# Kernel tuning notes

Measured on AMD Instinct MI355X. Metric: run time of the kernel, lower is better.

## Reference

```python
import jax, jax.numpy as jnp
import numpy as np

B, N, C, S, G, COOR = 4, 8192, 64, 2048, 32, 3
C2 = 2 * C            # channels after SetAbstraction
EXP = 4
RADII = (0.2, 0.4, 0.4)


def _sqdist(src, dst):
    # (B,M,3),(B,N,3) -> (B,M,N) squared distances (same expansion as torch code)
    d = -2.0 * jnp.einsum('bmc,bnc->bmn', src, dst)
    d = d + jnp.sum(src ** 2, -1)[:, :, None]
    d = d + jnp.sum(dst ** 2, -1)[:, None, :]
    return d


def _gather(points, idx):
    # points (B,N,C), idx (B,...) -> (B,...,C)
    return jax.vmap(lambda p, i: p[i])(points, idx)


def _fps(xyz, npoint):
    # xyz (B,N,3) -> (B,npoint) farthest point sample indices (start at index 0)
    b, n, _ = xyz.shape

    def step(carry, _):
        distance, farthest = carry
        centroid = jnp.take_along_axis(xyz, farthest[:, None, None], axis=1)  # (B,1,3)
        d = jnp.sqrt(jnp.sum((xyz - centroid) ** 2, -1))
        distance = jnp.minimum(distance, d)
        nxt = jnp.argmax(distance, -1)
        return (distance, nxt), farthest

    init = (jnp.full((b, n), 1e10, xyz.dtype), jnp.zeros((b,), jnp.int32))
    _, idxs = jax.lax.scan(step, init, None, length=npoint)
    return jnp.transpose(idxs)  # (B,npoint)


def _query_hybrid(radius, nsample, xyz, new_xyz):
    d = _sqdist(new_xyz, xyz)                       # (B,S,N)
    neg_d, idx = jax.lax.top_k(-d, nsample)         # smallest distances
    mask = (-neg_d) > radius ** 2
    first = idx[:, :, :1]
    return jnp.where(mask, first, idx)              # (B,S,nsample)


def _group(coor, new_coor, fea, radius, nsample):
    # coor (B,N,3), new_coor (B,S,3), fea (B,N,C) -> (B,S,G,C+3)
    gi = _query_hybrid(radius, nsample, coor, new_coor)
    gc = (_gather(coor, gi) - new_coor[:, :, None, :]) / radius
    gf = _gather(fea, gi)
    return jnp.concatenate([gf, gc], axis=-1)


def _mlp_max(g, w):
    # g (B,S,G,Cin), w (Cout,Cin): 1x1 conv (no bias) + ReLU, then max over group
    h = jax.nn.relu(jnp.einsum('bsgc,dc->bsgd', g, w))
    return jnp.max(h, axis=2)  # (B,S,Cout)


def _inv_res_mlp(coor, fea, radius, nsample, w_la, w1, w2):
    # coor (B,S,3), fea (B,S,C2) channels-last
    identity = fea
    g = _group(coor, coor, fea, radius, nsample)
    fea = _mlp_max(g, w_la)                              # LocalAggregation
    fea = jax.nn.relu(jnp.einsum('bsc,dc->bsd', fea, w1))
    fea = jnp.einsum('bsc,dc->bsd', fea, w2)             # last ReLU dropped
    return jax.nn.relu(fea + identity)


def setup_inputs() -> dict:
    key = jax.random.key(0)
    ks = jax.random.split(key, 10)
    def w(k, o, i):
        return jax.random.normal(k, (o, i), jnp.float32) / np.sqrt(i)
    return {
        'points_coor': jax.random.uniform(ks[0], (B, 3, N), jnp.float32),
        'points_fea': jax.random.normal(ks[1], (B, C, N), jnp.float32),
        'w_sa':  w(ks[2], C2, C + COOR),
        'w_la1': w(ks[3], C2, C2 + COOR),
        'w1_1':  w(ks[4], C2 * EXP, C2),
        'w2_1':  w(ks[5], C2, C2 * EXP),
        'w_la2': w(ks[6], C2, C2 + COOR),
        'w1_2':  w(ks[7], C2 * EXP, C2),
        'w2_2':  w(ks[8], C2, C2 * EXP),
    }


def reference(points_coor, points_fea, w_sa, w_la1, w1_1, w2_1, w_la2, w1_2, w2_2):
    coor = jnp.transpose(points_coor, (0, 2, 1))  # (B,N,3)
    fea = jnp.transpose(points_fea, (0, 2, 1))    # (B,N,C)
    # SetAbstraction: S-G-P
    fps_idx = _fps(coor, S)
    new_coor = _gather(coor, fps_idx)             # (B,S,3)
    g = _group(coor, new_coor, fea, RADII[0], G)
    new_fea = _mlp_max(g, w_sa)                   # (B,S,2C)
    # InvResMLP blocks
    new_fea = _inv_res_mlp(new_coor, new_fea, RADII[1], G, w_la1, w1_1, w2_1)
    new_fea = _inv_res_mlp(new_coor, new_fea, RADII[2], G, w_la2, w1_2, w2_2)
    return (jnp.transpose(new_coor, (0, 2, 1)), jnp.transpose(new_fea, (0, 2, 1)))
```

## Files before the change

kernel.cpp:

```cpp
#include <hip/hip_runtime.h>
#include <hip/hip_bf16.h>

#define BB 4
#define NN 8192
#define CC 64
#define SS 2048
#define GG 32
#define C2V 128
#define HHV 512

typedef unsigned long long u64;
typedef unsigned int u32;

__global__ void k_transpose_fea(const float* __restrict__ in, float* __restrict__ out) {
  __shared__ float tile[32][33];
  const int b = blockIdx.z;
  const int n0 = blockIdx.x * 32, c0 = blockIdx.y * 32;
  const int tx = threadIdx.x, ty = threadIdx.y;
  const float* src = in + (size_t)b * CC * NN;
#pragma unroll
  for (int i = 0; i < 32; i += 8)
    tile[ty + i][tx] = src[(size_t)(c0 + ty + i) * NN + n0 + tx];
  __syncthreads();
  float* dst = out + (size_t)b * NN * CC;
#pragma unroll
  for (int i = 0; i < 32; i += 8)
    dst[(size_t)(n0 + ty + i) * CC + c0 + tx] = tile[tx][ty + i];
}

__global__ __launch_bounds__(512) void k_fps(const float* __restrict__ pc, int* __restrict__ fps_idx) {
#pragma clang fp contract(off)
  const int b = blockIdx.x, tid = threadIdx.x;
  const int lane = tid & 63, wid = tid >> 6;
  const float* pb = pc + (size_t)b * 3 * NN;
  const float4* p4x = (const float4*)pb;
  const float4* p4y = (const float4*)(pb + NN);
  const float4* p4z = (const float4*)(pb + 2 * NN);
  float4 X0 = p4x[tid * 4 + 0], X1 = p4x[tid * 4 + 1], X2 = p4x[tid * 4 + 2], X3 = p4x[tid * 4 + 3];
  float4 Y0 = p4y[tid * 4 + 0], Y1 = p4y[tid * 4 + 1], Y2 = p4y[tid * 4 + 2], Y3 = p4y[tid * 4 + 3];
  float4 Z0 = p4z[tid * 4 + 0], Z1 = p4z[tid * 4 + 1], Z2 = p4z[tid * 4 + 2], Z3 = p4z[tid * 4 + 3];
  float4 D0 = make_float4(1e20f, 1e20f, 1e20f, 1e20f);
  float4 D1 = D0, D2q = D0, D3 = D0;

  __shared__ u64 sK[2][8];
  if (lane == 0)
    sK[0][wid] = (wid == 0) ? ((((u64)0xFFFFFFFFu) << 32) | (u64)0xFFFFFFFFu) : 0ull;
  __syncthreads();

#define DPPK64(K, CTL) { \
      u32 lo = (u32)(K), hi = (u32)((K) >> 32); \
      u32 lo2 = (u32)__builtin_amdgcn_update_dpp(0, (int)lo, CTL, 0xf, 0xf, false); \
      u32 hi2 = (u32)__builtin_amdgcn_update_dpp(0, (int)hi, CTL, 0xf, 0xf, false); \
      u64 k2 = ((u64)hi2 << 32) | (u64)lo2; if (k2 > (K)) (K) = k2; }
#define RMAXF(V, CTL) { \
      float t_ = __int_as_float(__builtin_amdgcn_update_dpp(0, __float_as_int(V), CTL, 0xf, 0xf, false)); \
      (V) = fmaxf((V), t_); }
#define RMINU(V, CTL) { \
      u32 t_ = (u32)__builtin_amdgcn_update_dpp(0, (int)(V), CTL, 0xf, 0xf, false); \
      (V) = min((V), t_); }

  for (int k = 0; k < SS; ++k) {
    const int p = k & 1;
    u64 kk = sK[p][lane & 7];
    DPPK64(kk, 0x121) DPPK64(kk, 0x122) DPPK64(kk, 0x124)
    const int g = (int)(0xFFFFFFFFu - (u32)kk);
    if (tid == 0) fps_idx[b * SS + k] = g;
    const float cx = pb[g], cy = pb[NN + g], cz = pb[2 * NN + g];

#define UPDC(XX, YY, ZZ, DD) { \
      float dx_ = (XX) - cx, dy_ = (YY) - cy, dz_ = (ZZ) - cz; \
      float t0_ = dx_ * dx_, t1_ = dy_ * dy_, t2_ = dz_ * dz_; \
      float s_ = (t0_ + t1_) + t2_; \
      (DD) = fminf((DD), s_); }
    UPDC(X0.x, Y0.x, Z0.x, D0.x) UPDC(X0.y, Y0.y, Z0.y, D0.y)
    UPDC(X0.z, Y0.z, Z0.z, D0.z) UPDC(X0.w, Y0.w, Z0.w, D0.w)
    UPDC(X1.x, Y1.x, Z1.x, D1.x) UPDC(X1.y, Y1.y, Z1.y, D1.y)
    UPDC(X1.z, Y1.z, Z1.z, D1.z) UPDC(X1.w, Y1.w, Z1.w, D1.w)
    UPDC(X2.x, Y2.x, Z2.x, D2q.x) UPDC(X2.y, Y2.y, Z2.y, D2q.y)
    UPDC(X2.z, Y2.z, Z2.z, D2q.z) UPDC(X2.w, Y2.w, Z2.w, D2q.w)
    UPDC(X3.x, Y3.x, Z3.x, D3.x) UPDC(X3.y, Y3.y, Z3.y, D3.y)
    UPDC(X3.z, Y3.z, Z3.z, D3.z) UPDC(X3.w, Y3.w, Z3.w, D3.w)
#undef UPDC

    float m2 = fmaxf(
        fmaxf(fmaxf(fmaxf(D0.x, D0.y), fmaxf(D0.z, D0.w)),
              fmaxf(fmaxf(D1.x, D1.y), fmaxf(D1.z, D1.w))),
        fmaxf(fmaxf(fmaxf(D2q.x, D2q.y), fmaxf(D2q.z, D2q.w)),
              fmaxf(fmaxf(D3.x, D3.y), fmaxf(D3.z, D3.w))));
    float s = sqrtf(m2);

    u32 sbits = __float_as_uint(s);
    float spred = __uint_as_float(sbits - 1u);
    double M = ((double)spred + (double)s) * 0.5;
    double L = M * M;
    if (sbits & 1u) L = __longlong_as_double(__double_as_longlong(L) + 1ll);
    float Lf = (float)L;
    if ((double)Lf < L) Lf = __uint_as_float(__float_as_uint(Lf) + 1u);

    int jsel = 0;
    jsel = (D3.w >= Lf) ? 15 : jsel; jsel = (D3.z >= Lf) ? 14 : jsel;
    jsel = (D3.y >= Lf) ? 13 : jsel; jsel = (D3.x >= Lf) ? 12 : jsel;
    jsel = (D2q.w >= Lf) ? 11 : jsel; jsel = (D2q.z >= Lf) ? 10 : jsel;
    jsel = (D2q.y >= Lf) ? 9 : jsel; jsel = (D2q.x >= Lf) ? 8 : jsel;
    jsel = (D1.w >= Lf) ? 7 : jsel; jsel = (D1.z >= Lf) ? 6 : jsel;
    jsel = (D1.y >= Lf) ? 5 : jsel; jsel = (D1.x >= Lf) ? 4 : jsel;
    jsel = (D0.w >= Lf) ? 3 : jsel; jsel = (D0.z >= Lf) ? 2 : jsel;
    jsel = (D0.y >= Lf) ? 1 : jsel; jsel = (D0.x >= Lf) ? 0 : jsel;

    float sm = s;
    RMAXF(sm, 0x121) RMAXF(sm, 0x122) RMAXF(sm, 0x124) RMAXF(sm, 0x128)
    sm = fmaxf(sm, __shfl_xor(sm, 16, 64));
    sm = fmaxf(sm, __shfl_xor(sm, 32, 64));
    u32 enc = (s == sm) ? (u32)(tid * 16 + jsel) : 0xFFFFFFFFu;
    RMINU(enc, 0x121) RMINU(enc, 0x122) RMINU(enc, 0x124) RMINU(enc, 0x128)
    enc = min(enc, (u32)__shfl_xor((int)enc, 16, 64));
    enc = min(enc, (u32)__shfl_xor((int)enc, 32, 64));

    u64 key = (((u64)__float_as_uint(sm)) << 32) | (u64)(0xFFFFFFFFu - enc);
    if (lane == 0) sK[p ^ 1][wid] = key;
    __syncthreads();
  }
#undef DPPK64
#undef RMAXF
#undef RMINU
}

__global__ void k_gather(const float* __restrict__ pc, const int* __restrict__ fps_idx,
                         float* __restrict__ ncoor, float* __restrict__ out0) {
  int t = blockIdx.x * 256 + threadIdx.x;
  if (t >= BB * SS) return;
  int b = t / SS, s = t % SS;
  int id = fps_idx[t];
  const float* base = pc + (size_t)b * 3 * NN;
  float x = base[id], y = base[NN + id], z = base[2 * NN + id];
  ncoor[(size_t)t * 3] = x; ncoor[(size_t)t * 3 + 1] = y; ncoor[(size_t)t * 3 + 2] = z;
  size_t o = (size_t)b * 3 * SS + s;
  out0[o] = x; out0[o + SS] = y; out0[o + 2 * SS] = z;
}

__global__ __launch_bounds__(256) void k_knn(const float* __restrict__ candp,
                                             const float* __restrict__ newc,
                                             int mode, int ncand, float r2,
                                             int* __restrict__ gidx) {
  __shared__ float cd[2048];
  __shared__ int ci[2048];
  __shared__ int hist[64];
  __shared__ int cnt, oc, binT, mlow;
  const int q = blockIdx.x, tid = threadIdx.x;
  const int b = q / SS;
  if (tid == 0) { cnt = 0; oc = 0; }
  if (tid < 64) hist[tid] = 0;
  __syncthreads();
  const float qx = newc[(size_t)q * 3], qy = newc[(size_t)q * 3 + 1], qz = newc[(size_t)q * 3 + 2];
  float qn;
  {
#pragma clang fp contract(off)
    qn = (qx * qx + qy * qy) + qz * qz;
  }
  const float sc = 64.0f / r2;
  const float* base = (mode == 0) ? candp + (size_t)b * 3 * NN : candp + (size_t)b * SS * 3;
  for (int i = tid; i < ncand; i += 256) {
    float x, y, z;
    if (mode == 0) { x = base[i]; y = base[NN + i]; z = base[2 * NN + i]; }
    else { x = base[3 * i]; y = base[3 * i + 1]; z = base[3 * i + 2]; }
    float dot = fmaf(qz, z, fmaf(qy, y, qx * x));
    float d;
    {
#pragma clang fp contract(off)
      float pn = (x * x + y * y) + z * z;
      d = ((-2.0f * dot) + qn) + pn;
    }
    if (d <= r2) {
      int pp = atomicAdd(&cnt, 1);
      if (pp < 2048) { cd[pp] = d; ci[pp] = i; }
      float db = (d > 0.0f) ? d : 0.0f;
      atomicAdd(&hist[min(63, (int)(db * sc))], 1);
    }
  }
  __syncthreads();
  const int M = min(cnt, 2048);
  if (tid == 0) {
    if (M > 32) {
      int c = 0, t = 0;
      for (t = 0; t < 64; ++t) { if (c + hist[t] >= 32) break; c += hist[t]; }
      binT = t; mlow = c;
    } else binT = -1;
  }
  __syncthreads();
  int* out = gidx + (size_t)q * 32;
  if (binT < 0) {
    for (int j = tid; j < M; j += 256) out[atomicAdd(&oc, 1)] = ci[j];
    __syncthreads();
    if (tid == 0 && M < 32) {
      float bd = 1e30f; int bx = 0x7FFFFFFF;
      for (int j = 0; j < M; ++j)
        if (cd[j] < bd || (cd[j] == bd && ci[j] < bx)) { bd = cd[j]; bx = ci[j]; }
      for (int j = M; j < 32; ++j) out[j] = bx;
    }
  } else {
    const int bt = binT, m = mlow;
    for (int j = tid; j < M; j += 256) {
      float dbj = (cd[j] > 0.0f) ? cd[j] : 0.0f;
      int bin = min(63, (int)(dbj * sc));
      if (bin < bt) out[atomicAdd(&oc, 1)] = ci[j];
      else if (bin == bt) {
        int r = 0; const float dj = cd[j]; const int ij = ci[j];
        for (int kk = 0; kk < M; ++kk) {
          float dbk = (cd[kk] > 0.0f) ? cd[kk] : 0.0f;
          if (min(63, (int)(dbk * sc)) == bt &&
              (cd[kk] < dj || (cd[kk] == dj && ci[kk] < ij))) ++r;
        }
        if (m + r < 32) out[m + r] = ci[j];
      }
    }
  }
}

template <int FDIM>
__global__ __launch_bounds__(256) void k_group_mlp(
    const float* __restrict__ fea, const int* __restrict__ gidx,
    const float* __restrict__ newc, const float* __restrict__ candp,
    int mode, int ncand, float radius,
    const float* __restrict__ wp, float* __restrict__ outf) {
  constexpr int CP4 = FDIM + 4;
  constexpr int NC4 = CP4 / 4;
  __shared__ float4 g4[2][32][NC4];
  __shared__ int sidx[2][32];
  __shared__ float sq[2][3];
  __shared__ float pf[2][4][128];
  const int tid = threadIdx.x;
  const int rs = tid >> 7, tl = tid & 127;
  const int dt = tl & 31, et = tl >> 5;
  const int d0 = dt * 4, e0 = et * 8;
  const int row0 = blockIdx.x * 16;
  for (int rp = 0; rp < 16; rp += 2) {
    const int row = row0 + rp + rs;
    if (tl < 32) sidx[rs][tl] = gidx[(size_t)row * 32 + tl];
    if (tl < 3) sq[rs][tl] = newc[(size_t)row * 3 + tl];
    __syncthreads();
    const int bb2 = row / SS;
    const float* fb = fea + (size_t)bb2 * ncand * FDIM;
    const float* cb = (mode == 0) ? candp + (size_t)bb2 * 3 * NN
                                  : candp + (size_t)bb2 * SS * 3;
    float* gf = (float*)&g4[rs][0][0];
    for (int qq = tl; qq < 32 * CP4; qq += 128) {
      int e = qq / CP4, c = qq - e * CP4;
      int id = sidx[rs][e];
      float v;
      if (c < FDIM) v = fb[(size_t)id * FDIM + c];
      else if (c < FDIM + 3) {
        int comp = c - FDIM;
        float pcv = (mode == 0) ? cb[(size_t)comp * NN + id] : cb[(size_t)id * 3 + comp];
        v = (pcv - sq[rs][comp]) / radius;
      } else v = 0.0f;
      gf[qq] = v;
    }
    __syncthreads();
    float acc[4][8];
#pragma unroll
    for (int i = 0; i < 4; ++i)
#pragma unroll
      for (int j = 0; j < 8; ++j) acc[i][j] = 0.0f;
    const float4* w4 = (const float4*)wp;
    for (int c4 = 0; c4 < NC4; ++c4) {
      float4 wv[4], gv[8];
#pragma unroll
      for (int i = 0; i < 4; ++i) wv[i] = w4[(size_t)(d0 + i) * NC4 + c4];
#pragma unroll
      for (int j = 0; j < 8; ++j) gv[j] = g4[rs][e0 + j][c4];
#pragma unroll
      for (int i = 0; i < 4; ++i)
#pragma unroll
        for (int j = 0; j < 8; ++j) {
          acc[i][j] += wv[i].x * gv[j].x;
          acc[i][j] += wv[i].y * gv[j].y;
          acc[i][j] += wv[i].z * gv[j].z;
          acc[i][j] += wv[i].w * gv[j].w;
        }
    }
#pragma unroll
    for (int i = 0; i < 4; ++i) {
      float m = acc[i][0];
#pragma unroll
      for (int j = 1; j < 8; ++j) m = fmaxf(m, acc[i][j]);
      pf[rs][et][d0 + i] = m;
    }
    __syncthreads();
    {
      const int d = tid & 127, r2s = tid >> 7;
      const int rowW = row0 + rp + r2s;
      float m = fmaxf(fmaxf(pf[r2s][0][d], pf[r2s][1][d]),
                      fmaxf(pf[r2s][2][d], pf[r2s][3][d]));
      outf[(size_t)rowW * 128 + d] = fmaxf(m, 0.0f);
    }
    __syncthreads();
  }
}

template <bool RESID>
__global__ __launch_bounds__(256) void k_dense(
    const float* __restrict__ A, const float* __restrict__ W,
    const float* __restrict__ Id, float* __restrict__ Out,
    int K, int Ntot) {
  __shared__ float4 sa[64][17], sb[64][17];
  const int m0 = blockIdx.x * 64, n0 = blockIdx.y * 64;
  const int tid = threadIdx.x;
  const int mt = tid & 15, nt = tid >> 4;
  float acc[4][4];
#pragma unroll
  for (int i = 0; i < 4; ++i)
#pragma unroll
    for (int j = 0; j < 4; ++j) acc[i][j] = 0.0f;
  for (int kc = 0; kc < K; kc += 64) {
    for (int q2 = tid; q2 < 2048; q2 += 256) {
      int half = q2 >> 10, qq = q2 & 1023;
      int r = qq >> 4, c = qq & 15;
      const float* src = half ? (W + (size_t)(n0 + r) * K + kc + c * 4)
                              : (A + (size_t)(m0 + r) * K + kc + c * 4);
      float4 v = *(const float4*)src;
      if (half) sb[r][c] = v; else sa[r][c] = v;
    }
    __syncthreads();
#pragma unroll
    for (int c = 0; c < 16; ++c) {
      const int ks = (c + mt + nt) & 15;
      float4 av[4], bv[4];
#pragma unroll
      for (int i = 0; i < 4; ++i) av[i] = sa[mt * 4 + i][ks];
#pragma unroll
      for (int j = 0; j < 4; ++j) bv[j] = sb[nt * 4 + j][ks];
#pragma unroll
      for (int i = 0; i < 4; ++i)
#pragma unroll
        for (int j = 0; j < 4; ++j) {
          acc[i][j] += av[i].x * bv[j].x;
          acc[i][j] += av[i].y * bv[j].y;
          acc[i][j] += av[i].z * bv[j].z;
          acc[i][j] += av[i].w * bv[j].w;
        }
    }
    __syncthreads();
  }
#pragma unroll
  for (int i = 0; i < 4; ++i)
#pragma unroll
    for (int j = 0; j < 4; ++j) {
      size_t o = (size_t)(m0 + mt * 4 + i) * Ntot + n0 + nt * 4 + j;
      float v = acc[i][j];
      if (RESID) v += Id[o];
      Out[o] = fmaxf(v, 0.0f);
    }
}

__global__ void k_pad_w(const float* __restrict__ src, float* __restrict__ dst,
                        int rows, int cin, int cp4) {
  int t = blockIdx.x * 256 + threadIdx.x;
  if (t >= rows * cp4) return;
  int r = t / cp4, c = t - r * cp4;
  dst[t] = (c < cin) ? src[(size_t)r * cin + c] : 0.0f;
}

__global__ void k_out1_t(const float* __restrict__ in, float* __restrict__ out) {
  __shared__ float tile[32][33];
  const int b = blockIdx.z;
  const int s0 = blockIdx.x * 32, d0 = blockIdx.y * 32;
  const int tx = threadIdx.x, ty = threadIdx.y;
#pragma unroll
  for (int i = 0; i < 32; i += 8)
    tile[ty + i][tx] = in[(size_t)(b * SS + s0 + ty + i) * 128 + d0 + tx];
  __syncthreads();
#pragma unroll
  for (int i = 0; i < 32; i += 8)
    out[(size_t)(b * 128 + d0 + ty + i) * SS + s0 + tx] = tile[tx][ty + i];
}

extern "C" void kernel_launch(void* const* d_in, const int* in_sizes, int n_in,
                              void* d_out, int out_size, void* d_ws, size_t ws_size,
                              hipStream_t stream) {
  const float* pc    = (const float*)d_in[0];
  const float* pfea  = (const float*)d_in[1];
  const float* w_sa  = (const float*)d_in[2];
  const float* w_la1 = (const float*)d_in[3];
  const float* w1_1  = (const float*)d_in[4];
  const float* w2_1  = (const float*)d_in[5];
  const float* w_la2 = (const float*)d_in[6];
  const float* w1_2  = (const float*)d_in[7];
  const float* w2_2  = (const float*)d_in[8];
  float* out0 = (float*)d_out;
  float* out1 = out0 + (size_t)BB * 3 * SS;

  char* wsp = (char*)d_ws;
  size_t off = 0;
  auto alloc = [&](size_t bytes) -> void* {
    void* p = wsp + off;
    off = (off + bytes + 255) & ~(size_t)255;
    return p;
  };
  float* hbuf = (float*)alloc((size_t)BB * SS * HHV * 4);
  float* feaT = hbuf;
  int*   fpsi = (int*)alloc((size_t)BB * SS * 4);
  float* ncoor = (float*)alloc((size_t)BB * SS * 3 * 4);
  int*   gi = (int*)alloc((size_t)BB * SS * GG * 4);
  float* fa = (float*)alloc((size_t)BB * SS * C2V * 4);
  float* fb = (float*)alloc((size_t)BB * SS * C2V * 4);
  float* wsap = (float*)alloc(128 * 68 * 4);
  float* wla1p = (float*)alloc(128 * 132 * 4);
  float* wla2p = (float*)alloc(128 * 132 * 4);

  k_pad_w<<<dim3((128 * 68 + 255) / 256), dim3(256), 0, stream>>>(w_sa, wsap, 128, 67, 68);
  k_pad_w<<<dim3((128 * 132 + 255) / 256), dim3(256), 0, stream>>>(w_la1, wla1p, 128, 131, 132);
  k_pad_w<<<dim3((128 * 132 + 255) / 256), dim3(256), 0, stream>>>(w_la2, wla2p, 128, 131, 132);

  k_transpose_fea<<<dim3(NN / 32, CC / 32, BB), dim3(32, 8), 0, stream>>>(pfea, feaT);
  k_fps<<<dim3(BB), dim3(512), 0, stream>>>(pc, fpsi);
  k_gather<<<dim3((BB * SS + 255) / 256), dim3(256), 0, stream>>>(pc, fpsi, ncoor, out0);

  k_knn<<<dim3(BB * SS), dim3(256), 0, stream>>>(pc, ncoor, 0, NN, 0.04f, gi);
  k_group_mlp<64><<<dim3(BB * SS / 16), dim3(256), 0, stream>>>(feaT, gi, ncoor, pc, 0, NN, 0.2f, wsap, fa);

  k_knn<<<dim3(BB * SS), dim3(256), 0, stream>>>(ncoor, ncoor, 1, SS, 0.16f, gi);

  k_group_mlp<128><<<dim3(BB * SS / 16), dim3(256), 0, stream>>>(fa, gi, ncoor, ncoor, 1, SS, 0.4f, wla1p, fb);
  k_dense<false><<<dim3(128, 8), dim3(256), 0, stream>>>(fb, w1_1, nullptr, hbuf, 128, 512);
  k_dense<true><<<dim3(128, 2), dim3(256), 0, stream>>>(hbuf, w2_1, fa, fb, 512, 128);

  k_group_mlp<128><<<dim3(BB * SS / 16), dim3(256), 0, stream>>>(fb, gi, ncoor, ncoor, 1, SS, 0.4f, wla2p, fa);
  k_dense<false><<<dim3(128, 8), dim3(256), 0, stream>>>(fa, w1_2, nullptr, hbuf, 128, 512);
  k_dense<true><<<dim3(128, 2), dim3(256), 0, stream>>>(hbuf, w2_2, fb, fa, 512, 128);

  k_out1_t<<<dim3(SS / 32, 128 / 32, BB), dim3(32, 8), 0, stream>>>(fa, out1);
}
```

Baseline: 4.061 ms.

## Pass FPS winner coordinates via shared memory and compute sub-index only in winning lane

The FPS loop now has the winning thread of each wave write the selected point's coordinates and index into shared memory next to its key. Every lane then fetches the centroid with a shuffle instead of a dependent global load. The per-element argmax selection and threshold computation now run only in the lane holding the wave max, rather than in every lane before the reduction. The launch bounds also request two blocks per CU. This is meant to remove global-memory latency and redundant ALU work from the serial critical path, at the cost of divergent code in one lane and possible register pressure under the tighter launch bound.

```diff
diff --git a/kernel.cpp b/kernel.cpp
--- a/kernel.cpp
+++ b/kernel.cpp
@@ -28,7 +28,7 @@
     dst[(size_t)(n0 + ty + i) * CC + c0 + tx] = tile[tx][ty + i];
 }
 
-__global__ __launch_bounds__(512) void k_fps(const float* __restrict__ pc, int* __restrict__ fps_idx) {
+__global__ __launch_bounds__(512, 2) void k_fps(const float* __restrict__ pc, int* __restrict__ fps_idx) {
 #pragma clang fp contract(off)
   const int b = blockIdx.x, tid = threadIdx.x;
   const int lane = tid & 63, wid = tid >> 6;
@@ -43,8 +43,12 @@
   float4 D1 = D0, D2q = D0, D3 = D0;
 
   __shared__ u64 sK[2][8];
-  if (lane == 0)
-    sK[0][wid] = (wid == 0) ? ((((u64)0xFFFFFFFFu) << 32) | (u64)0xFFFFFFFFu) : 0ull;
+  __shared__ float4 sC[2][8];
+  if (lane == 0) sK[0][wid] = 0ull;
+  if (tid == 0) {
+    sK[0][0] = ~0ull;
+    sC[0][0] = make_float4(X0.x, Y0.x, Z0.x, __int_as_float(0));
+  }
   __syncthreads();
 
 #define DPPK64(K, CTL) { \
@@ -60,12 +64,16 @@
       (V) = min((V), t_); }
 
   for (int k = 0; k < SS; ++k) {
-    const int p = k & 1;
+    const int p = k & 1, pn = p ^ 1;
     u64 kk = sK[p][lane & 7];
+    float4 cw = sC[p][lane & 7];
     DPPK64(kk, 0x121) DPPK64(kk, 0x122) DPPK64(kk, 0x124)
-    const int g = (int)(0xFFFFFFFFu - (u32)kk);
-    if (tid == 0) fps_idx[b * SS + k] = g;
-    const float cx = pb[g], cy = pb[NN + g], cz = pb[2 * NN + g];
+    const int wslot = (int)((0xFFFFFFFFu - (u32)kk) >> 6);
+    const float cx = __shfl(cw.x, wslot, 64);
+    const float cy = __shfl(cw.y, wslot, 64);
+    const float cz = __shfl(cw.z, wslot, 64);
+    const float gw = __shfl(cw.w, wslot, 64);
+    if (tid == 0) fps_idx[b * SS + k] = __float_as_int(gw);
 
 #define UPDC(XX, YY, ZZ, DD) { \
       float dx_ = (XX) - cx, dy_ = (YY) - cy, dz_ = (ZZ) - cz; \
@@ -89,35 +97,38 @@
               fmaxf(fmaxf(D3.x, D3.y), fmaxf(D3.z, D3.w))));
     float s = sqrtf(m2);
 
-    u32 sbits = __float_as_uint(s);
-    float spred = __uint_as_float(sbits - 1u);
-    double M = ((double)spred + (double)s) * 0.5;
-    double L = M * M;
-    if (sbits & 1u) L = __longlong_as_double(__double_as_longlong(L) + 1ll);
-    float Lf = (float)L;
-    if ((double)Lf < L) Lf = __uint_as_float(__float_as_uint(Lf) + 1u);
-
-    int jsel = 0;
-    jsel = (D3.w >= Lf) ? 15 : jsel; jsel = (D3.z >= Lf) ? 14 : jsel;
-    jsel = (D3.y >= Lf) ? 13 : jsel; jsel = (D3.x >= Lf) ? 12 : jsel;
-    jsel = (D2q.w >= Lf) ? 11 : jsel; jsel = (D2q.z >= Lf) ? 10 : jsel;
-    jsel = (D2q.y >= Lf) ? 9 : jsel; jsel = (D2q.x >= Lf) ? 8 : jsel;
-    jsel = (D1.w >= Lf) ? 7 : jsel; jsel = (D1.z >= Lf) ? 6 : jsel;
-    jsel = (D1.y >= Lf) ? 5 : jsel; jsel = (D1.x >= Lf) ? 4 : jsel;
-    jsel = (D0.w >= Lf) ? 3 : jsel; jsel = (D0.z >= Lf) ? 2 : jsel;
-    jsel = (D0.y >= Lf) ? 1 : jsel; jsel = (D0.x >= Lf) ? 0 : jsel;
-
     float sm = s;
     RMAXF(sm, 0x121) RMAXF(sm, 0x122) RMAXF(sm, 0x124) RMAXF(sm, 0x128)
     sm = fmaxf(sm, __shfl_xor(sm, 16, 64));
     sm = fmaxf(sm, __shfl_xor(sm, 32, 64));
-    u32 enc = (s == sm) ? (u32)(tid * 16 + jsel) : 0xFFFFFFFFu;
-    RMINU(enc, 0x121) RMINU(enc, 0x122) RMINU(enc, 0x124) RMINU(enc, 0x128)
-    enc = min(enc, (u32)__shfl_xor((int)enc, 16, 64));
-    enc = min(enc, (u32)__shfl_xor((int)enc, 32, 64));
-
-    u64 key = (((u64)__float_as_uint(sm)) << 32) | (u64)(0xFFFFFFFFu - enc);
-    if (lane == 0) sK[p ^ 1][wid] = key;
+    u32 encT = (s == sm) ? (u32)tid : 0xFFFFFFFFu;
+    RMINU(encT, 0x121) RMINU(encT, 0x122) RMINU(encT, 0x124) RMINU(encT, 0x128)
+    encT = min(encT, (u32)__shfl_xor((int)encT, 16, 64));
+    encT = min(encT, (u32)__shfl_xor((int)encT, 32, 64));
+
+    if ((u32)tid == encT) {
+      u32 sbits = __float_as_uint(s);
+      float spred = __uint_as_float(sbits - 1u);
+      double M = ((double)spred + (double)s) * 0.5;
+      double L = M * M;
+      if (sbits & 1u) L = __longlong_as_double(__double_as_longlong(L) + 1ll);
+      float Lf = (float)L;
+      if ((double)Lf < L) Lf = __uint_as_float(__float_as_uint(Lf) + 1u);
+
+      int jsel = 15; float sx = X3.w, sy = Y3.w, sz = Z3.w;
+#define SELC(J, DD, XX, YY, ZZ) if ((DD) >= Lf) { jsel = J; sx = (XX); sy = (YY); sz = (ZZ); }
+      SELC(14, D3.z, X3.z, Y3.z, Z3.z) SELC(13, D3.y, X3.y, Y3.y, Z3.y)
+      SELC(12, D3.x, X3.x, Y3.x, Z3.x) SELC(11, D2q.w, X2.w, Y2.w, Z2.w)
+      SELC(10, D2q.z, X2.z, Y2.z, Z2.z) SELC(9, D2q.y, X2.y, Y2.y, Z2.y)
+      SELC(8, D2q.x, X2.x, Y2.x, Z2.x) SELC(7, D1.w, X1.w, Y1.w, Z1.w)
+      SELC(6, D1.z, X1.z, Y1.z, Z1.z) SELC(5, D1.y, X1.y, Y1.y, Z1.y)
+      SELC(4, D1.x, X1.x, Y1.x, Z1.x) SELC(3, D0.w, X0.w, Y0.w, Z0.w)
+      SELC(2, D0.z, X0.z, Y0.z, Z0.z) SELC(1, D0.y, X0.y, Y0.y, Z0.y)
+      SELC(0, D0.x, X0.x, Y0.x, Z0.x)
+#undef SELC
+      sK[pn][wid] = (((u64)__float_as_uint(s)) << 32) | (u64)(0xFFFFFFFFu - (u32)tid);
+      sC[pn][wid] = make_float4(sx, sy, sz, __int_as_float(tid * 16 + jsel));
+    }
     __syncthreads();
   }
 #undef DPPK64
```

After: 4.720 ms. 16.2% more time.

## Widen FPS to 1024 threads with LDS-resident coordinates and lazy argmax tie-break

Applied to the files above, without the earlier changes.

The farthest-point-sampling kernel now runs 1024 threads per batch instead of 512, so each thread owns 8 points instead of 16. Coordinates are staged in shared memory rather than held in registers, and the centroid is read from LDS instead of global memory. The expensive double-precision threshold and index-selection step now runs only in lanes that hold the wave max. This shortens the per-iteration serial chain of the single-block-per-batch loop, at the cost of LDS reads every iteration, a 16-wave barrier, and one extra DPP reduction step.

```diff
diff --git a/kernel.cpp b/kernel.cpp
--- a/kernel.cpp
+++ b/kernel.cpp
@@ -28,24 +28,30 @@
     dst[(size_t)(n0 + ty + i) * CC + c0 + tx] = tile[tx][ty + i];
 }
 
-__global__ __launch_bounds__(512) void k_fps(const float* __restrict__ pc, int* __restrict__ fps_idx) {
+__global__ __launch_bounds__(1024, 4) void k_fps(const float* __restrict__ pc, int* __restrict__ fps_idx) {
 #pragma clang fp contract(off)
+  __shared__ float lx[NN], ly[NN], lz[NN];
+  __shared__ u64 sK[2][16];
   const int b = blockIdx.x, tid = threadIdx.x;
   const int lane = tid & 63, wid = tid >> 6;
   const float* pb = pc + (size_t)b * 3 * NN;
-  const float4* p4x = (const float4*)pb;
-  const float4* p4y = (const float4*)(pb + NN);
-  const float4* p4z = (const float4*)(pb + 2 * NN);
-  float4 X0 = p4x[tid * 4 + 0], X1 = p4x[tid * 4 + 1], X2 = p4x[tid * 4 + 2], X3 = p4x[tid * 4 + 3];
-  float4 Y0 = p4y[tid * 4 + 0], Y1 = p4y[tid * 4 + 1], Y2 = p4y[tid * 4 + 2], Y3 = p4y[tid * 4 + 3];
-  float4 Z0 = p4z[tid * 4 + 0], Z1 = p4z[tid * 4 + 1], Z2 = p4z[tid * 4 + 2], Z3 = p4z[tid * 4 + 3];
+  {
+    const float4* gx = (const float4*)pb;
+    const float4* gy = (const float4*)(pb + NN);
+    const float4* gz = (const float4*)(pb + 2 * NN);
+    float4* sx = (float4*)lx; float4* sy = (float4*)ly; float4* sz = (float4*)lz;
+    sx[tid] = gx[tid]; sx[tid + 1024] = gx[tid + 1024];
+    sy[tid] = gy[tid]; sy[tid + 1024] = gy[tid + 1024];
+    sz[tid] = gz[tid]; sz[tid + 1024] = gz[tid + 1024];
+  }
+  if (tid < 32) ((u64*)sK)[tid] = 0ull;
+  if (tid == 0) sK[0][0] = ~0ull;
+  __syncthreads();
+
+  const int fbase = wid * 64 + lane;
+  const u32 ibase = (u32)(wid * 256 + lane * 4);
   float4 D0 = make_float4(1e20f, 1e20f, 1e20f, 1e20f);
-  float4 D1 = D0, D2q = D0, D3 = D0;
-
-  __shared__ u64 sK[2][8];
-  if (lane == 0)
-    sK[0][wid] = (wid == 0) ? ((((u64)0xFFFFFFFFu) << 32) | (u64)0xFFFFFFFFu) : 0ull;
-  __syncthreads();
+  float4 D1 = D0;
 
 #define DPPK64(K, CTL) { \
       u32 lo = (u32)(K), hi = (u32)((K) >> 32); \
@@ -60,64 +66,62 @@
       (V) = min((V), t_); }
 
   for (int k = 0; k < SS; ++k) {
-    const int p = k & 1;
-    u64 kk = sK[p][lane & 7];
-    DPPK64(kk, 0x121) DPPK64(kk, 0x122) DPPK64(kk, 0x124)
-    const int g = (int)(0xFFFFFFFFu - (u32)kk);
-    if (tid == 0) fps_idx[b * SS + k] = g;
-    const float cx = pb[g], cy = pb[NN + g], cz = pb[2 * NN + g];
+    const int p = k & 1, pn = p ^ 1;
+    u64 kk = sK[p][lane & 15];
+    DPPK64(kk, 0x121) DPPK64(kk, 0x122) DPPK64(kk, 0x124) DPPK64(kk, 0x128)
+    const u32 idx = 0xFFFFFFFFu - (u32)kk;
+    if (tid == 0) fps_idx[b * SS + k] = (int)idx;
+    const float cx = lx[idx], cy = ly[idx], cz = lz[idx];
+
+    const float4 Xa = ((const float4*)lx)[fbase], Xb = ((const float4*)lx)[fbase + 1024];
+    const float4 Ya = ((const float4*)ly)[fbase], Yb = ((const float4*)ly)[fbase + 1024];
+    const float4 Za = ((const float4*)lz)[fbase], Zb = ((const float4*)lz)[fbase + 1024];
 
 #define UPDC(XX, YY, ZZ, DD) { \
       float dx_ = (XX) - cx, dy_ = (YY) - cy, dz_ = (ZZ) - cz; \
       float t0_ = dx_ * dx_, t1_ = dy_ * dy_, t2_ = dz_ * dz_; \
       float s_ = (t0_ + t1_) + t2_; \
       (DD) = fminf((DD), s_); }
-    UPDC(X0.x, Y0.x, Z0.x, D0.x) UPDC(X0.y, Y0.y, Z0.y, D0.y)
-    UPDC(X0.z, Y0.z, Z0.z, D0.z) UPDC(X0.w, Y0.w, Z0.w, D0.w)
-    UPDC(X1.x, Y1.x, Z1.x, D1.x) UPDC(X1.y, Y1.y, Z1.y, D1.y)
-    UPDC(X1.z, Y1.z, Z1.z, D1.z) UPDC(X1.w, Y1.w, Z1.w, D1.w)
-    UPDC(X2.x, Y2.x, Z2.x, D2q.x) UPDC(X2.y, Y2.y, Z2.y, D2q.y)
-    UPDC(X2.z, Y2.z, Z2.z, D2q.z) UPDC(X2.w, Y2.w, Z2.w, D2q.w)
-    UPDC(X3.x, Y3.x, Z3.x, D3.x) UPDC(X3.y, Y3.y, Z3.y, D3.y)
-    UPDC(X3.z, Y3.z, Z3.z, D3.z) UPDC(X3.w, Y3.w, Z3.w, D3.w)
+    UPDC(Xa.x, Ya.x, Za.x, D0.x) UPDC(Xa.y, Ya.y, Za.y, D0.y)
+    UPDC(Xa.z, Ya.z, Za.z, D0.z) UPDC(Xa.w, Ya.w, Za.w, D0.w)
+    UPDC(Xb.x, Yb.x, Zb.x, D1.x) UPDC(Xb.y, Yb.y, Zb.y, D1.y)
+    UPDC(Xb.z, Yb.z, Zb.z, D1.z) UPDC(Xb.w, Yb.w, Zb.w, D1.w)
 #undef UPDC
 
-    float m2 = fmaxf(
-        fmaxf(fmaxf(fmaxf(D0.x, D0.y), fmaxf(D0.z, D0.w)),
-              fmaxf(fmaxf(D1.x, D1.y), fmaxf(D1.z, D1.w))),
-        fmaxf(fmaxf(fmaxf(D2q.x, D2q.y), fmaxf(D2q.z, D2q.w)),
-              fmaxf(fmaxf(D3.x, D3.y), fmaxf(D3.z, D3.w))));
+    float m2 = fmaxf(fmaxf(fmaxf(D0.x, D0.y), fmaxf(D0.z, D0.w)),
+                     fmaxf(fmaxf(D1.x, D1.y), fmaxf(D1.z, D1.w)));
     float s = sqrtf(m2);
-
-    u32 sbits = __float_as_uint(s);
-    float spred = __uint_as_float(sbits - 1u);
-    double M = ((double)spred + (double)s) * 0.5;
-    double L = M * M;
-    if (sbits & 1u) L = __longlong_as_double(__double_as_longlong(L) + 1ll);
-    float Lf = (float)L;
-    if ((double)Lf < L) Lf = __uint_as_float(__float_as_uint(Lf) + 1u);
-
-    int jsel = 0;
-    jsel = (D3.w >= Lf) ? 15 : jsel; jsel = (D3.z >= Lf) ? 14 : jsel;
-    jsel = (D3.y >= Lf) ? 13 : jsel; jsel = (D3.x >= Lf) ? 12 : jsel;
-    jsel = (D2q.w >= Lf) ? 11 : jsel; jsel = (D2q.z >= Lf) ? 10 : jsel;
-    jsel = (D2q.y >= Lf) ? 9 : jsel; jsel = (D2q.x >= Lf) ? 8 : jsel;
-    jsel = (D1.w >= Lf) ? 7 : jsel; jsel = (D1.z >= Lf) ? 6 : jsel;
-    jsel = (D1.y >= Lf) ? 5 : jsel; jsel = (D1.x >= Lf) ? 4 : jsel;
-    jsel = (D0.w >= Lf) ? 3 : jsel; jsel = (D0.z >= Lf) ? 2 : jsel;
-    jsel = (D0.y >= Lf) ? 1 : jsel; jsel = (D0.x >= Lf) ? 0 : jsel;
 
     float sm = s;
     RMAXF(sm, 0x121) RMAXF(sm, 0x122) RMAXF(sm, 0x124) RMAXF(sm, 0x128)
     sm = fmaxf(sm, __shfl_xor(sm, 16, 64));
     sm = fmaxf(sm, __shfl_xor(sm, 32, 64));
-    u32 enc = (s == sm) ? (u32)(tid * 16 + jsel) : 0xFFFFFFFFu;
+
+    u32 enc = 0xFFFFFFFFu;
+    if (s == sm) {
+      u32 sbits = __float_as_uint(sm);
+      float spred = __uint_as_float(sbits - 1u);
+      double M = ((double)spred + (double)sm) * 0.5;
+      double L = M * M;
+      if (sbits & 1u) L = __longlong_as_double(__double_as_longlong(L) + 1ll);
+      float Lf = (float)L;
+      if ((double)Lf < L) Lf = __uint_as_float(__float_as_uint(Lf) + 1u);
+      int off = 4096 + 3;
+      if (D1.z >= Lf) off = 4096 + 2;
+      if (D1.y >= Lf) off = 4096 + 1;
+      if (D1.x >= Lf) off = 4096 + 0;
+      if (D0.w >= Lf) off = 3;
+      if (D0.z >= Lf) off = 2;
+      if (D0.y >= Lf) off = 1;
+      if (D0.x >= Lf) off = 0;
+      enc = ibase + (u32)off;
+    }
     RMINU(enc, 0x121) RMINU(enc, 0x122) RMINU(enc, 0x124) RMINU(enc, 0x128)
     enc = min(enc, (u32)__shfl_xor((int)enc, 16, 64));
     enc = min(enc, (u32)__shfl_xor((int)enc, 32, 64));
 
-    u64 key = (((u64)__float_as_uint(sm)) << 32) | (u64)(0xFFFFFFFFu - enc);
-    if (lane == 0) sK[p ^ 1][wid] = key;
+    if (lane == 0)
+      sK[pn][wid] = (((u64)__float_as_uint(sm)) << 32) | (u64)(0xFFFFFFFFu - enc);
     __syncthreads();
   }
 #undef DPPK64
@@ -412,7 +416,7 @@
   k_pad_w<<<dim3((128 * 132 + 255) / 256), dim3(256), 0, stream>>>(w_la2, wla2p, 128, 131, 132);
 
   k_transpose_fea<<<dim3(NN / 32, CC / 32, BB), dim3(32, 8), 0, stream>>>(pfea, feaT);
-  k_fps<<<dim3(BB), dim3(512), 0, stream>>>(pc, fpsi);
+  k_fps<<<dim3(BB), dim3(1024), 0, stream>>>(pc, fpsi);
   k_gather<<<dim3((BB * SS + 255) / 256), dim3(256), 0, stream>>>(pc, fpsi, ncoor, out0);
 
   k_knn<<<dim3(BB * SS), dim3(256), 0, stream>>>(pc, ncoor, 0, NN, 0.04f, gi);
```

Result: slower. 4.287 ms, median of 2 (+5.6%).
